# Kernel optimization log

Measured on AMD Instinct MI355X. Metric: run time of the kernel, lower is better.

The kernel has to match this reference:

```python
import jax, jax.numpy as jnp
import numpy as np

D, H1, H2, OUT = 1024, 4096, 4096, 1


def _tanh_jet(a0, a1, a2):
    # 2nd-order Taylor-mode push-through of tanh:
    # u0 = tanh(a0); u1 = sech^2(a0)*a1; u2 = sech^2(a0)*a2 - 2*tanh(a0)*sech^2(a0)*a1^2
    u0 = jnp.tanh(a0)
    s = 1.0 - u0 * u0
    u1 = s * a1
    u2 = s * a2 - 2.0 * u0 * s * (a1 * a1)
    return u0, u1, u2


def setup_inputs() -> dict:
    key = jax.random.key(0)
    ks = jax.random.split(key, 7)
    x = jax.random.normal(ks[0], (D,), dtype=jnp.float32)
    # Kaiming-like scaling so tanh stays in its nonlinear regime
    W1 = jax.random.normal(ks[1], (H1, D), dtype=jnp.float32) / np.sqrt(D)
    b1 = jax.random.normal(ks[2], (H1,), dtype=jnp.float32) * 0.01
    W2 = jax.random.normal(ks[3], (H2, H1), dtype=jnp.float32) / np.sqrt(H1)
    b2 = jax.random.normal(ks[4], (H2,), dtype=jnp.float32) * 0.01
    W3 = jax.random.normal(ks[5], (OUT, H2), dtype=jnp.float32) / np.sqrt(H2)
    b3 = jax.random.normal(ks[6], (OUT,), dtype=jnp.float32) * 0.01
    return {"x": x, "W1": W1, "b1": b1, "W2": W2, "b2": b2, "W3": W3, "b3": b3}


def reference(x, W1, b1, W2, b2, W3, b3):
    # propagated simultaneously over all D basis tangent vectors (vectorized vmap).
    d = x.shape[0]
    X1 = jnp.eye(d, dtype=x.dtype)            # [D, D] basis tangents; x2 = 0
    # layer 1 (linear): primal broadcasts over the tangent batch
    a0 = x @ W1.T + b1                         # [H1]
    a1 = X1 @ W1.T                             # [D, H1]
    a2 = jnp.zeros_like(a1)                    # second input coefficient is zero
    u0, u1, u2 = _tanh_jet(a0, a1, a2)
    # layer 2 (linear)
    z0 = u0 @ W2.T + b2                        # [H2]
    z1 = u1 @ W2.T                             # [D, H2]
    z2 = u2 @ W2.T                             # [D, H2]
    v0, v1, v2 = _tanh_jet(z0, z1, z2)
    # layer 3 (linear); F2[i] = e_i^T H_f(x) e_i
    F2 = v2 @ W3.T                             # [D, 1]
    return F2.sum(0)                           # [1] = trace(H_f) = Laplacian
```

## Files before the change

kernel.cpp:

```cpp
#include <hip/hip_runtime.h>
#include <math.h>

#define DD 1024
#define HH1 4096
#define HH2 4096

typedef __attribute__((ext_vector_type(8))) short bf16x8;
typedef __attribute__((ext_vector_type(4))) float f32x4;
typedef unsigned short ushort_t;

#define WS_FAST_BYTES 42008576ull
#define K4_LDS_BYTES (131072 + 64)

__device__ inline void wave_reduce2(float& a, float& b) {
  #pragma unroll
  for (int off = 32; off > 0; off >>= 1) {
    a += __shfl_down(a, off, 64);
    b += __shfl_down(b, off, 64);
  }
}

__device__ inline unsigned int f2b(float f) {
  union { float f; unsigned int u; } v; v.f = f;
  return (v.u + 0x7FFFu + ((v.u >> 16) & 1u)) >> 16;
}
__device__ inline unsigned int pack2(float a, float b) {
  return f2b(a) | (f2b(b) << 16);
}

__device__ inline void gl_lds16(const void* g, void* l) {
  __builtin_amdgcn_global_load_lds(
      (const __attribute__((address_space(1))) unsigned int*)g,
      (__attribute__((address_space(3))) unsigned int*)l, 16, 0, 0);
}

#define TP2 1032
__global__ __launch_bounds__(256) void kA3_l1t(
    const float* __restrict__ W1, const float* __restrict__ x,
    const float* __restrict__ b1, float* __restrict__ u0,
    float* __restrict__ q, ushort_t* __restrict__ Bp) {
  __shared__ __align__(16) ushort_t T[16 * TP2];
  const int tid = threadIdx.x;
  const int h0 = blockIdx.x * 16;
  const int r = tid >> 4;
  const int c = tid & 15;
  const float4* rp = (const float4*)(W1 + (size_t)(h0 + r) * DD);
  const float4* x4 = (const float4*)x;
  float dot = 0.f, sq = 0.f;
  #pragma unroll
  for (int j = 0; j < 16; ++j) {
    const int f = c + j * 16;
    float4 wv = rp[f];
    float4 xv = x4[f];
    dot += wv.x * xv.x + wv.y * xv.y + wv.z * xv.z + wv.w * xv.w;
    sq  += wv.x * wv.x + wv.y * wv.y + wv.z * wv.z + wv.w * wv.w;
    uint2 pk;
    pk.x = pack2(wv.x, wv.y);
    pk.y = pack2(wv.z, wv.w);
    *(uint2*)&T[r * TP2 + f * 4] = pk;
  }
  #pragma unroll
  for (int off = 8; off > 0; off >>= 1) {
    dot += __shfl_down(dot, off, 16);
    sq  += __shfl_down(sq, off, 16);
  }
  if (c == 0) {
    float a0 = dot + b1[h0 + r];
    float u = tanhf(a0);
    float s = 1.f - u * u;
    u0[h0 + r] = u;
    q[h0 + r] = -2.f * u * s * sq;
  }
  __syncthreads();
  #pragma unroll
  for (int rep = 0; rep < 2; ++rep) {
    const int ip = rep * 512 + tid * 2;
    #pragma unroll
    for (int cg = 0; cg < 2; ++cg) {
      unsigned int R[8];
      #pragma unroll
      for (int r8 = 0; r8 < 8; ++r8)
        R[r8] = *(const unsigned int*)&T[(cg * 8 + r8) * TP2 + ip];
      unsigned int oa[4], ob[4];
      #pragma unroll
      for (int k2 = 0; k2 < 4; ++k2) {
        oa[k2] = (R[2 * k2] & 0xffffu) | (R[2 * k2 + 1] << 16);
        ob[k2] = (R[2 * k2] >> 16) | (R[2 * k2 + 1] & 0xffff0000u);
      }
      *(uint4*)(Bp + (size_t)ip * HH1 + h0 + cg * 8) = *(const uint4*)oa;
      *(uint4*)(Bp + (size_t)(ip + 1) * HH1 + h0 + cg * 8) = *(const uint4*)ob;
    }
  }
}

__global__ __launch_bounds__(256) void k0a_layer2conv(
    const float* __restrict__ W2, const float* __restrict__ b2,
    const float* __restrict__ W3, const float* __restrict__ u0,
    const float* __restrict__ q, ushort_t* __restrict__ Ap,
    float* __restrict__ cv, float* __restrict__ cd) {
  int g = blockIdx.x;
  int tid = threadIdx.x;
  const float4* row = (const float4*)(W2 + (size_t)g * HH1);
  const float4* u4 = (const float4*)u0;
  const float4* q4 = (const float4*)q;
  float4 w[4], u[4], qq[4];
  #pragma unroll
  for (int it = 0; it < 4; ++it) w[it] = row[tid + it * 256];
  #pragma unroll
  for (int it = 0; it < 4; ++it) u[it] = u4[tid + it * 256];
  #pragma unroll
  for (int it = 0; it < 4; ++it) qq[it] = q4[tid + it * 256];
  float zacc = 0.f, dacc = 0.f;
  #pragma unroll
  for (int it = 0; it < 4; ++it) {
    const int j = tid + it * 256;
    float4 sv;
    sv.x = 1.f - u[it].x * u[it].x;
    sv.y = 1.f - u[it].y * u[it].y;
    sv.z = 1.f - u[it].z * u[it].z;
    sv.w = 1.f - u[it].w * u[it].w;
    zacc += w[it].x * u[it].x + w[it].y * u[it].y +
            w[it].z * u[it].z + w[it].w * u[it].w;
    dacc += w[it].x * qq[it].x + w[it].y * qq[it].y +
            w[it].z * qq[it].z + w[it].w * qq[it].w;
    uint2 pk;
    pk.x = pack2(w[it].x * sv.x, w[it].y * sv.y);
    pk.y = pack2(w[it].z * sv.z, w[it].w * sv.w);
    *(uint2*)(Ap + (size_t)g * HH1 + j * 4) = pk;
  }
  wave_reduce2(zacc, dacc);
  __shared__ float lds[8];
  int lane = tid & 63, wid = tid >> 6;
  if (lane == 0) { lds[wid * 2] = zacc; lds[wid * 2 + 1] = dacc; }
  __syncthreads();
  if (tid == 0) {
    float z = lds[0] + lds[2] + lds[4] + lds[6] + b2[g];
    float d = lds[1] + lds[3] + lds[5] + lds[7];
    float v = tanhf(z);
    float t = 1.f - v * v;
    float c = W3[g] * t;
    cv[g] = c * v;
    cd[g] = c * d;
  }
}

__global__ __launch_bounds__(512) void k4_bt64q(
    const ushort_t* __restrict__ Ap, const ushort_t* __restrict__ Bp,
    const float* __restrict__ cv, float* __restrict__ P) {
  extern __shared__ __align__(16) char smem[];
  char* const Ab0 = smem;
  char* const Bb0 = smem + 65536;
  float* const red = (float*)(smem + 131072);

  const int tid = threadIdx.x;
  const int lane = tid & 63;
  const int wave = tid >> 6;
  const int wm = wave >> 1;
  const int wn = wave & 1;
  const int l = blockIdx.x;
  const int xcd = l & 7;
  const int jj = l >> 3;
  const int g0 = (xcd * 4 + (jj & 3)) * 128;
  const int i0 = (jj >> 2) * 128;

  const int srow = lane >> 3;
  const int schunk = (lane & 7) ^ srow;
  const size_t agbase = (size_t)(g0 + srow) * HH1 + schunk * 8;
  const size_t bgbase = (size_t)(i0 + srow) * HH1 + schunk * 8;

  const int fr = lane & 15;
  const int fc = lane >> 4;
  const int rsw = fr & 7;

  f32x4 acc[2][4];
  const f32x4 zero = {0.f, 0.f, 0.f, 0.f};
  #pragma unroll
  for (int mt = 0; mt < 2; ++mt)
    #pragma unroll
    for (int nt = 0; nt < 4; ++nt) acc[mt][nt] = zero;

  #define STAGE_PAIR(tile, sub) do {                                        \
      const int buf_ = (tile) & 3;                                          \
      const int r0_ = wave * 16 + (sub) * 8;                                \
      const size_t koff_ = (size_t)(((tile) & 63) * 64);                    \
      gl_lds16(Ap + agbase + (size_t)r0_ * HH1 + koff_,                     \
               Ab0 + buf_ * 16384 + r0_ * 128);                             \
      gl_lds16(Bp + bgbase + (size_t)r0_ * HH1 + koff_,                     \
               Bb0 + buf_ * 16384 + r0_ * 128);                             \
    } while (0)

  STAGE_PAIR(0, 0); STAGE_PAIR(0, 1);
  STAGE_PAIR(1, 0); STAGE_PAIR(1, 1);
  STAGE_PAIR(2, 0); STAGE_PAIR(2, 1);

  for (int t = 0; t < 64; ++t) {
    const int buf = t & 3;
    const char* Abuf = Ab0 + buf * 16384;
    const char* Bbuf = Bb0 + buf * 16384;
    asm volatile("s_waitcnt vmcnt(8)" ::: "memory");
    __builtin_amdgcn_s_barrier();
    asm volatile("" ::: "memory");
    #pragma unroll
    for (int kk = 0; kk < 2; ++kk) {
      STAGE_PAIR(t + 3, kk);
      bf16x8 af[2], bfv[4];
      #pragma unroll
      for (int mt = 0; mt < 2; ++mt) {
        const int row = wm * 32 + mt * 16 + fr;
        af[mt] = *(const bf16x8*)(Abuf + row * 128 + (((kk * 4 + fc) ^ rsw) * 16));
      }
      #pragma unroll
      for (int nt = 0; nt < 4; ++nt) {
        const int row = wn * 64 + nt * 16 + fr;
        bfv[nt] = *(const bf16x8*)(Bbuf + row * 128 + (((kk * 4 + fc) ^ rsw) * 16));
      }
      __builtin_amdgcn_s_setprio(1);
      #pragma unroll
      for (int mt = 0; mt < 2; ++mt)
        #pragma unroll
        for (int nt = 0; nt < 4; ++nt)
          acc[mt][nt] = __builtin_amdgcn_mfma_f32_16x16x32_bf16(
              af[mt], bfv[nt], acc[mt][nt], 0, 0, 0);
      __builtin_amdgcn_s_setprio(0);
      if (kk == 0) __builtin_amdgcn_s_barrier();
    }
  }
  #undef STAGE_PAIR

  float part = 0.f;
  #pragma unroll
  for (int mt = 0; mt < 2; ++mt) {
    #pragma unroll
    for (int r = 0; r < 4; ++r) {
      const int g = g0 + wm * 32 + mt * 16 + fc * 4 + r;
      const float c = cv[g];
      float ss = 0.f;
      #pragma unroll
      for (int nt = 0; nt < 4; ++nt) {
        float v = acc[mt][nt][r];
        ss += v * v;
      }
      part += c * ss;
    }
  }
  #pragma unroll
  for (int off = 32; off > 0; off >>= 1) part += __shfl_down(part, off, 64);
  if (lane == 0) red[wave] = part;
  __syncthreads();
  if (tid == 0) {
    float s = 0.f;
    #pragma unroll
    for (int w2 = 0; w2 < 8; ++w2) s += red[w2];
    P[l] = s;
  }
}

__global__ __launch_bounds__(256) void k5_final(
    const float* __restrict__ cd, const float* __restrict__ P,
    float* __restrict__ out) {
  int tid = threadIdx.x;
  float a = 0.f;
  for (int j = tid; j < HH2; j += 256) a += cd[j];
  float b = P[tid];
  float v = a - 2.f * b;
  #pragma unroll
  for (int off = 32; off > 0; off >>= 1) v += __shfl_down(v, off, 64);
  __shared__ float lds[4];
  int lane = tid & 63, wid = tid >> 6;
  if (lane == 0) lds[wid] = v;
  __syncthreads();
  if (tid == 0) out[0] = lds[0] + lds[1] + lds[2] + lds[3];
}


__global__ __launch_bounds__(256) void k1_slow(
    const float* __restrict__ W1, const float* __restrict__ x,
    const float* __restrict__ b1, float* __restrict__ u0,
    float* __restrict__ q, float* __restrict__ s_out,
    float* __restrict__ out) {
  int h = blockIdx.x;
  int tid = threadIdx.x;
  const float4* row = (const float4*)(W1 + (size_t)h * DD);
  const float4* x4 = (const float4*)x;
  float4 w = row[tid];
  float4 xv = x4[tid];
  float dot = w.x * xv.x + w.y * xv.y + w.z * xv.z + w.w * xv.w;
  float sq = w.x * w.x + w.y * w.y + w.z * w.z + w.w * w.w;
  wave_reduce2(dot, sq);
  __shared__ float lds[8];
  int lane = tid & 63, wid = tid >> 6;
  if (lane == 0) { lds[wid * 2] = dot; lds[wid * 2 + 1] = sq; }
  __syncthreads();
  if (tid == 0) {
    float dsum = lds[0] + lds[2] + lds[4] + lds[6];
    float rsum = lds[1] + lds[3] + lds[5] + lds[7];
    float a0 = dsum + b1[h];
    float u = tanhf(a0);
    float s = 1.f - u * u;
    u0[h] = u;
    s_out[h] = s;
    q[h] = -2.f * u * s * rsum;
    if (h == 0) out[0] = 0.f;
  }
}

__global__ __launch_bounds__(256) void k2_slow(
    const float* __restrict__ W2, const float* __restrict__ b2,
    const float* __restrict__ W3, const float* __restrict__ u0,
    const float* __restrict__ q, float* __restrict__ cv,
    float* __restrict__ out) {
  int g = blockIdx.x;
  int tid = threadIdx.x;
  const float4* row = (const float4*)(W2 + (size_t)g * HH1);
  const float4* u4 = (const float4*)u0;
  const float4* q4 = (const float4*)q;
  float zacc = 0.f, dacc = 0.f;
  for (int j = tid; j < HH1 / 4; j += 256) {
    float4 w = row[j];
    float4 u = u4[j];
    float4 qq = q4[j];
    zacc += w.x * u.x + w.y * u.y + w.z * u.z + w.w * u.w;
    dacc += w.x * qq.x + w.y * qq.y + w.z * qq.z + w.w * qq.w;
  }
  wave_reduce2(zacc, dacc);
  __shared__ float lds[8];
  int lane = tid & 63, wid = tid >> 6;
  if (lane == 0) { lds[wid * 2] = zacc; lds[wid * 2 + 1] = dacc; }
  __syncthreads();
  if (tid == 0) {
    float z = lds[0] + lds[2] + lds[4] + lds[6] + b2[g];
    float d = lds[1] + lds[3] + lds[5] + lds[7];
    float v = tanhf(z);
    float t = 1.f - v * v;
    float c = W3[g] * t;
    cv[g] = c * v;
    atomicAdd(out, c * d);
  }
}

__global__ __launch_bounds__(256) void k4_slow(
    const float* __restrict__ W2, const float* __restrict__ W1,
    const float* __restrict__ s, const float* __restrict__ cv,
    float* __restrict__ out) {
  __shared__ float As[32][68];
  __shared__ float Bs[32][68];
  int tid = threadIdx.x;
  int g0 = blockIdx.y * 64;
  int i0 = blockIdx.x * 64;
  int tr = (tid / 16) * 4;
  int tc = (tid % 16) * 4;
  float acc[4][4] = {};
  for (int k0 = 0; k0 < HH1; k0 += 32) {
    for (int ll = tid; ll < (64 * 32 / 4); ll += 256) {
      int row = ll / 8;
      int c4 = ll % 8;
      float4 w = *(const float4*)(W2 + (size_t)(g0 + row) * HH1 + k0 + c4 * 4);
      float4 sv = *(const float4*)(s + k0 + c4 * 4);
      As[c4 * 4 + 0][row] = w.x * sv.x;
      As[c4 * 4 + 1][row] = w.y * sv.y;
      As[c4 * 4 + 2][row] = w.z * sv.z;
      As[c4 * 4 + 3][row] = w.w * sv.w;
    }
    for (int ll = tid; ll < (32 * 64 / 4); ll += 256) {
      int row = ll / 16;
      int c4 = ll % 16;
      float4 w = *(const float4*)(W1 + (size_t)(k0 + row) * DD + i0 + c4 * 4);
      *(float4*)&Bs[row][c4 * 4] = w;
    }
    __syncthreads();
    #pragma unroll
    for (int k = 0; k < 32; ++k) {
      float4 av = *(const float4*)&As[k][tr];
      float4 bv = *(const float4*)&Bs[k][tc];
      float a_[4] = {av.x, av.y, av.z, av.w};
      float b_[4] = {bv.x, bv.y, bv.z, bv.w};
      #pragma unroll
      for (int r = 0; r < 4; ++r)
        #pragma unroll
        for (int c = 0; c < 4; ++c)
          acc[r][c] += a_[r] * b_[c];
    }
    __syncthreads();
  }
  float contrib = 0.f;
  #pragma unroll
  for (int r = 0; r < 4; ++r) {
    float ss = acc[r][0] * acc[r][0] + acc[r][1] * acc[r][1] +
               acc[r][2] * acc[r][2] + acc[r][3] * acc[r][3];
    contrib += cv[g0 + tr + r] * ss;
  }
  #pragma unroll
  for (int off = 32; off > 0; off >>= 1) contrib += __shfl_down(contrib, off, 64);
  __shared__ float red[4];
  int lane = tid & 63, wid = tid >> 6;
  if (lane == 0) red[wid] = contrib;
  __syncthreads();
  if (tid == 0) atomicAdd(out, -2.f * (red[0] + red[1] + red[2] + red[3]));
}

extern "C" void kernel_launch(void* const* d_in, const int* in_sizes, int n_in,
                              void* d_out, int out_size, void* d_ws, size_t ws_size,
                              hipStream_t stream) {
  const float* x  = (const float*)d_in[0];
  const float* W1 = (const float*)d_in[1];
  const float* b1 = (const float*)d_in[2];
  const float* W2 = (const float*)d_in[3];
  const float* b2 = (const float*)d_in[4];
  const float* W3 = (const float*)d_in[5];
  float* out = (float*)d_out;
  float* ws = (float*)d_ws;

  if (ws_size >= WS_FAST_BYTES) {
    float* u0 = ws;
    float* q  = ws + 4096;
    float* cv = ws + 8192;
    float* cd = ws + 12288;
    float* P  = ws;
    ushort_t* Ap = (ushort_t*)((char*)d_ws + 65536);
    ushort_t* Bp = (ushort_t*)((char*)d_ws + 33619968);
    hipFuncSetAttribute((const void*)k4_bt64q,
                        hipFuncAttributeMaxDynamicSharedMemorySize,
                        K4_LDS_BYTES);
    hipLaunchKernelGGL(kA3_l1t, dim3(256), dim3(256), 0, stream,
                       W1, x, b1, u0, q, Bp);
    hipLaunchKernelGGL(k0a_layer2conv, dim3(HH2), dim3(256), 0, stream,
                       W2, b2, W3, u0, q, Ap, cv, cd);
    hipLaunchKernelGGL(k4_bt64q, dim3(256), dim3(512), K4_LDS_BYTES, stream,
                       Ap, Bp, cv, P);
    hipLaunchKernelGGL(k5_final, dim3(1), dim3(256), 0, stream, cd, P, out);
  } else {
    float* u0 = ws;
    float* q  = ws + 4096;
    float* s  = ws + 8192;
    float* cv = ws + 12288;
    hipLaunchKernelGGL(k1_slow, dim3(HH1), dim3(256), 0, stream,
                       W1, x, b1, u0, q, s, out);
    hipLaunchKernelGGL(k2_slow, dim3(HH2), dim3(256), 0, stream,
                       W2, b2, W3, u0, q, cv, out);
    hipLaunchKernelGGL(k4_slow, dim3(DD / 64, HH2 / 64), dim3(256), 0, stream,
                       W2, W1, s, cv, out);
  }
}
```

Measured before the change: 171.2 us.

## Split GEMM K-loop across two wave groups with larger per-wave tiles

Restructures the main bf16 MFMA kernel so its 8 waves form two groups of 4. Each group processes alternate K tiles with a 64x64 per-wave output tile (4x4 MFMAs) instead of 32x64. The two groups' partial accumulators are summed through LDS at the end. Staging now loads two tiles per iteration with one barrier pair, cutting barriers per K step and raising MFMA-to-LDS-read ratio. In exchange it doubles accumulator registers, adds an LDS cross-group reduction, and leaves only half the waves for the final epilogue.

```diff
diff --git a/kernel.cpp b/kernel.cpp
--- a/kernel.cpp
+++ b/kernel.cpp
@@ -10,7 +10,7 @@
 typedef unsigned short ushort_t;
 
 #define WS_FAST_BYTES 42008576ull
-#define K4_LDS_BYTES (131072 + 64)
+#define K4_LDS_BYTES 131072
 
 __device__ inline void wave_reduce2(float& a, float& b) {
   #pragma unroll
@@ -144,19 +144,17 @@
   }
 }
 
-__global__ __launch_bounds__(512) void k4_bt64q(
+__global__ __launch_bounds__(512) void k4_v4(
     const ushort_t* __restrict__ Ap, const ushort_t* __restrict__ Bp,
     const float* __restrict__ cv, float* __restrict__ P) {
   extern __shared__ __align__(16) char smem[];
-  char* const Ab0 = smem;
-  char* const Bb0 = smem + 65536;
-  float* const red = (float*)(smem + 131072);
 
   const int tid = threadIdx.x;
   const int lane = tid & 63;
   const int wave = tid >> 6;
-  const int wm = wave >> 1;
-  const int wn = wave & 1;
+  const int gp = wave >> 2;
+  const int wq = wave & 3;
+  const int wm = wq >> 1, wn = wq & 1;
   const int l = blockIdx.x;
   const int xcd = l & 7;
   const int jj = l >> 3;
@@ -164,94 +162,113 @@
   const int i0 = (jj >> 2) * 128;
 
   const int srow = lane >> 3;
-  const int schunk = (lane & 7) ^ srow;
-  const size_t agbase = (size_t)(g0 + srow) * HH1 + schunk * 8;
-  const size_t bgbase = (size_t)(i0 + srow) * HH1 + schunk * 8;
+  const int lchunk = (lane & 7) ^ srow;
+  const ushort_t* gA0 = Ap + (size_t)(g0 + wave * 16 + 0 + srow) * HH1 + lchunk * 8;
+  const ushort_t* gA1 = Ap + (size_t)(g0 + wave * 16 + 8 + srow) * HH1 + lchunk * 8;
+  const ushort_t* gB0 = Bp + (size_t)(i0 + wave * 16 + 0 + srow) * HH1 + lchunk * 8;
+  const ushort_t* gB1 = Bp + (size_t)(i0 + wave * 16 + 8 + srow) * HH1 + lchunk * 8;
 
   const int fr = lane & 15;
   const int fc = lane >> 4;
   const int rsw = fr & 7;
 
-  f32x4 acc[2][4];
+  f32x4 acc[4][4];
   const f32x4 zero = {0.f, 0.f, 0.f, 0.f};
   #pragma unroll
-  for (int mt = 0; mt < 2; ++mt)
+  for (int mt = 0; mt < 4; ++mt)
     #pragma unroll
     for (int nt = 0; nt < 4; ++nt) acc[mt][nt] = zero;
 
-  #define STAGE_PAIR(tile, sub) do {                                        \
-      const int buf_ = (tile) & 3;                                          \
-      const int r0_ = wave * 16 + (sub) * 8;                                \
-      const size_t koff_ = (size_t)(((tile) & 63) * 64);                    \
-      gl_lds16(Ap + agbase + (size_t)r0_ * HH1 + koff_,                     \
-               Ab0 + buf_ * 16384 + r0_ * 128);                             \
-      gl_lds16(Bp + bgbase + (size_t)r0_ * HH1 + koff_,                     \
-               Bb0 + buf_ * 16384 + r0_ * 128);                             \
+  #define STAGE(tile) do {                                              \
+      char* tb_ = smem + ((tile) & 3) * 32768;                          \
+      const int ko_ = ((tile) & 63) * 64;                               \
+      gl_lds16(gA0 + ko_, tb_ + (wave * 16 + 0) * 128 + lane * 16);     \
+      gl_lds16(gA1 + ko_, tb_ + (wave * 16 + 8) * 128 + lane * 16);     \
+      gl_lds16(gB0 + ko_, tb_ + 16384 + (wave * 16 + 0) * 128 + lane * 16); \
+      gl_lds16(gB1 + ko_, tb_ + 16384 + (wave * 16 + 8) * 128 + lane * 16); \
     } while (0)
 
-  STAGE_PAIR(0, 0); STAGE_PAIR(0, 1);
-  STAGE_PAIR(1, 0); STAGE_PAIR(1, 1);
-  STAGE_PAIR(2, 0); STAGE_PAIR(2, 1);
-
-  for (int t = 0; t < 64; ++t) {
-    const int buf = t & 3;
-    const char* Abuf = Ab0 + buf * 16384;
-    const char* Bbuf = Bb0 + buf * 16384;
+  STAGE(0); STAGE(1);
+  for (int s = 0; s < 32; ++s) {
+    STAGE(2 * s + 2);
+    STAGE(2 * s + 3);
     asm volatile("s_waitcnt vmcnt(8)" ::: "memory");
     __builtin_amdgcn_s_barrier();
     asm volatile("" ::: "memory");
+    const char* tb = smem + ((2 * s + gp) & 3) * 32768;
     #pragma unroll
     for (int kk = 0; kk < 2; ++kk) {
-      STAGE_PAIR(t + 3, kk);
-      bf16x8 af[2], bfv[4];
-      #pragma unroll
-      for (int mt = 0; mt < 2; ++mt) {
-        const int row = wm * 32 + mt * 16 + fr;
-        af[mt] = *(const bf16x8*)(Abuf + row * 128 + (((kk * 4 + fc) ^ rsw) * 16));
-      }
-      #pragma unroll
-      for (int nt = 0; nt < 4; ++nt) {
-        const int row = wn * 64 + nt * 16 + fr;
-        bfv[nt] = *(const bf16x8*)(Bbuf + row * 128 + (((kk * 4 + fc) ^ rsw) * 16));
-      }
+      const int cb = ((kk * 4 + fc) ^ rsw) * 16;
+      bf16x8 af[4], bfv[4];
+      #pragma unroll
+      for (int mt = 0; mt < 4; ++mt)
+        af[mt] = *(const bf16x8*)(tb + (wm * 64 + mt * 16 + fr) * 128 + cb);
+      #pragma unroll
+      for (int nt = 0; nt < 4; ++nt)
+        bfv[nt] = *(const bf16x8*)(tb + 16384 + (wn * 64 + nt * 16 + fr) * 128 + cb);
       __builtin_amdgcn_s_setprio(1);
       #pragma unroll
-      for (int mt = 0; mt < 2; ++mt)
+      for (int mt = 0; mt < 4; ++mt)
         #pragma unroll
         for (int nt = 0; nt < 4; ++nt)
           acc[mt][nt] = __builtin_amdgcn_mfma_f32_16x16x32_bf16(
               af[mt], bfv[nt], acc[mt][nt], 0, 0, 0);
       __builtin_amdgcn_s_setprio(0);
-      if (kk == 0) __builtin_amdgcn_s_barrier();
-    }
-  }
-  #undef STAGE_PAIR
-
+    }
+    asm volatile("" ::: "memory");
+    __builtin_amdgcn_s_barrier();
+  }
+  #undef STAGE
+
+  asm volatile("s_waitcnt vmcnt(0)" ::: "memory");
+  __builtin_amdgcn_s_barrier();
+
+  char* xz = smem + 65536 + wq * 16384;
+  if (gp == 1) {
+    #pragma unroll
+    for (int mt = 0; mt < 4; ++mt)
+      #pragma unroll
+      for (int nt = 0; nt < 4; ++nt)
+        *(f32x4*)(xz + (mt * 4 + nt) * 1024 + lane * 16) = acc[mt][nt];
+  }
+  __syncthreads();
   float part = 0.f;
-  #pragma unroll
-  for (int mt = 0; mt < 2; ++mt) {
-    #pragma unroll
-    for (int r = 0; r < 4; ++r) {
-      const int g = g0 + wm * 32 + mt * 16 + fc * 4 + r;
-      const float c = cv[g];
-      float ss = 0.f;
+  if (gp == 0) {
+    #pragma unroll
+    for (int mt = 0; mt < 4; ++mt) {
       #pragma unroll
       for (int nt = 0; nt < 4; ++nt) {
-        float v = acc[mt][nt][r];
-        ss += v * v;
+        f32x4 v = *(const f32x4*)(xz + (mt * 4 + nt) * 1024 + lane * 16);
+        acc[mt][nt][0] += v[0];
+        acc[mt][nt][1] += v[1];
+        acc[mt][nt][2] += v[2];
+        acc[mt][nt][3] += v[3];
       }
-      part += c * ss;
-    }
-  }
-  #pragma unroll
-  for (int off = 32; off > 0; off >>= 1) part += __shfl_down(part, off, 64);
-  if (lane == 0) red[wave] = part;
+    }
+    #pragma unroll
+    for (int mt = 0; mt < 4; ++mt) {
+      #pragma unroll
+      for (int r = 0; r < 4; ++r) {
+        const int g = g0 + wm * 64 + mt * 16 + fc * 4 + r;
+        const float c = cv[g];
+        float ss = 0.f;
+        #pragma unroll
+        for (int nt = 0; nt < 4; ++nt) {
+          float v = acc[mt][nt][r];
+          ss += v * v;
+        }
+        part += c * ss;
+      }
+    }
+    #pragma unroll
+    for (int off = 32; off > 0; off >>= 1) part += __shfl_down(part, off, 64);
+  }
+  __syncthreads();
+  if (gp == 0 && lane == 0) ((float*)smem)[wq] = part;
   __syncthreads();
   if (tid == 0) {
-    float s = 0.f;
-    #pragma unroll
-    for (int w2 = 0; w2 < 8; ++w2) s += red[w2];
-    P[l] = s;
+    float* rp = (float*)smem;
+    P[l] = rp[0] + rp[1] + rp[2] + rp[3];
   }
 }
 
@@ -418,14 +435,14 @@
     float* P  = ws;
     ushort_t* Ap = (ushort_t*)((char*)d_ws + 65536);
     ushort_t* Bp = (ushort_t*)((char*)d_ws + 33619968);
-    hipFuncSetAttribute((const void*)k4_bt64q,
+    hipFuncSetAttribute((const void*)k4_v4,
                         hipFuncAttributeMaxDynamicSharedMemorySize,
                         K4_LDS_BYTES);
     hipLaunchKernelGGL(kA3_l1t, dim3(256), dim3(256), 0, stream,
                        W1, x, b1, u0, q, Bp);
     hipLaunchKernelGGL(k0a_layer2conv, dim3(HH2), dim3(256), 0, stream,
                        W2, b2, W3, u0, q, Ap, cv, cd);
-    hipLaunchKernelGGL(k4_bt64q, dim3(256), dim3(512), K4_LDS_BYTES, stream,
+    hipLaunchKernelGGL(k4_v4, dim3(256), dim3(512), K4_LDS_BYTES, stream,
                        Ap, Bp, cv, P);
     hipLaunchKernelGGL(k5_final, dim3(1), dim3(256), 0, stream, cd, P, out);
   } else {
```

Result: slower. 175.0 us (+2.2%).
